# Performance work log

Hardware: AMD Instinct MI355X
Metric: run time of the kernel (lower is better)

The kernel has to match this reference:

```python
import jax, jax.numpy as jnp
import numpy as np


def _gumbel(key, shape):
    # -log(Exp(1)) == standard Gumbel; matches torch's -empty.exponential_().log()
    u = jax.random.uniform(key, shape, minval=1e-10, maxval=1.0)
    return -jnp.log(-jnp.log(u))


def setup_inputs() -> dict:
    key = jax.random.key(0)
    dims = [(1026, 1024), (3074, 1024), (5122, 512)]
    names = ['wc1', 'wc2', 'wd1', 'wd2', 'gc1', 'gc2', 'gd1', 'gd2']
    inp = {}
    k = key
    for li, (din, dout) in enumerate(dims, start=1):
        for nm in names:
            k, sub = jax.random.split(k)
            if nm.startswith('w'):
                inp[f'l{li}_{nm}'] = jax.random.normal(sub, (din, dout), dtype=jnp.float32)
            else:
                inp[f'l{li}_{nm}'] = _gumbel(sub, (din, dout)).astype(jnp.float32)
    k, kx, kw = jax.random.split(k, 3)
    inp['x'] = jax.random.uniform(kx, (32768, 512), dtype=jnp.float32)
    inp['lin_w'] = jax.random.uniform(kw, (1, 1024), dtype=jnp.float32)
    inp['tau'] = 1
    return inp


def _st_gate(w, g, tau):
    # hard gumbel-softmax over axis 0 with straight-through estimator
    y = jax.nn.softmax((w + g) / tau, axis=0)
    hard = jax.nn.one_hot(jnp.argmax(y, axis=0), w.shape[0], dtype=y.dtype).T
    return hard + y - jax.lax.stop_gradient(y)


def _logic_layer(h, ws, gs, tau, skip):
    wc1, wc2, wd1, wd2 = ws
    gc1, gc2, gd1, gd2 = gs
    c = (h @ _st_gate(wc1, gc1, tau)) * (h @ _st_gate(wc2, gc2, tau))  # AND
    a = h @ _st_gate(wd1, gd1, tau)
    b = h @ _st_gate(wd2, gd2, tau)
    d = 1.0 - (1.0 - a) * (1.0 - b)  # OR
    parts = [h, c, d] if skip else [c, d]
    return jnp.concatenate(parts, axis=-1)


def reference(x, l1_wc1, l1_wc2, l1_wd1, l1_wd2, l1_gc1, l1_gc2, l1_gd1, l1_gd2,
              l2_wc1, l2_wc2, l2_wd1, l2_wd2, l2_gc1, l2_gc2, l2_gd1, l2_gd2,
              l3_wc1, l3_wc2, l3_wd1, l3_wd2, l3_gc1, l3_gc2, l3_gd1, l3_gd2,
              lin_w, tau):
    t = jnp.asarray(tau, dtype=x.dtype)
    B = x.shape[0]
    # InputAugmentor: [x, 1-x, 1, 0]
    h = jnp.concatenate([x, 1.0 - x, jnp.ones((B, 1), x.dtype), jnp.zeros((B, 1), x.dtype)], axis=-1)
    layers = [
        ((l1_wc1, l1_wc2, l1_wd1, l1_wd2), (l1_gc1, l1_gc2, l1_gd1, l1_gd2), True),
        ((l2_wc1, l2_wc2, l2_wd1, l2_wd2), (l2_gc1, l2_gc2, l2_gd1, l2_gd2), True),
        ((l3_wc1, l3_wc2, l3_wd1, l3_wd2), (l3_gc1, l3_gc2, l3_gd1, l3_gd2), False),
    ]
    for ws, gs, skip in layers:
        h = _logic_layer(h, ws, gs, t, skip)
    # nonnegative == False -> weight used as-is
    return (h @ lin_w.T).squeeze(-1)
```

## Files before the change

### kernel.cpp

```cpp
#include <hip/hip_runtime.h>
#include <stdint.h>


struct GatePtrs {
    const float* w[12];
    const float* g[12];
};

__global__ __launch_bounds__(256) void argmax_kernel(GatePtrs gp,
                                                     unsigned long long* __restrict__ packed) {
    const int dins[3]  = {1026, 3074, 5122};
    const int douts[3] = {1024, 1024, 512};
    const int offs[3]  = {0, 4096, 8192};
    int gate  = blockIdx.z;
    int layer = gate >> 2;
    int din  = dins[layer];
    int dout = douts[layer];
    int c2 = blockIdx.x * 256 + threadIdx.x;
    int r0 = blockIdx.y * 64;
    if (2 * c2 >= dout || r0 >= din) return;
    int r1 = min(r0 + 64, din);
    const float* __restrict__ w = gp.w[gate];
    const float* __restrict__ g = gp.g[gate];
    float bx = -3.4e38f, by = -3.4e38f;
    int rx = r0, ry = r0;
    #pragma unroll 8
    for (int i = r0; i < r1; ++i) {
        float2 wv = *(const float2*)(w + (size_t)i * dout + 2 * c2);
        float2 gv = *(const float2*)(g + (size_t)i * dout + 2 * c2);
        float vx = wv.x + gv.x, vy = wv.y + gv.y;
        if (vx > bx) { bx = vx; rx = i; }
        if (vy > by) { by = vy; ry = i; }
    }
    unsigned long long* dst = packed + offs[layer] + (gate & 3) * dout + 2 * c2;
    unsigned int ux = __float_as_uint(bx);
    unsigned int kx = ux ^ ((ux & 0x80000000u) ? 0xFFFFFFFFu : 0x80000000u);
    atomicMax(dst, ((unsigned long long)kx << 32)
                   | (unsigned long long)(0xFFFFFFFFu - (unsigned int)rx));
    unsigned int uy = __float_as_uint(by);
    unsigned int ky = uy ^ ((uy & 0x80000000u) ? 0xFFFFFFFFu : 0x80000000u);
    atomicMax(dst + 1, ((unsigned long long)ky << 32)
                   | (unsigned long long)(0xFFFFFFFFu - (unsigned int)ry));
}

__global__ __launch_bounds__(256) void convert_kernel(const unsigned long long* __restrict__ packed,
                                                      uint2* __restrict__ pairs) {
    int i = blockIdx.x * 256 + threadIdx.x;
    if (i >= 5120) return;
    int l    = (i < 2048) ? 0 : ((i < 4096) ? 1 : 2);
    int half = (l == 2) ? 512 : 1024;
    int r    = i - l * 2048;
    int type = (r >= half) ? 1 : 0;
    int g    = r - type * half;
    int o1   = l * 4096 + 2 * type * half + g;
    int o2   = o1 + half;
    unsigned int i1 = 0xFFFFFFFFu - (unsigned int)(packed[o1] & 0xFFFFFFFFull);
    unsigned int i2 = 0xFFFFFFFFu - (unsigned int)(packed[o2] & 0xFFFFFFFFull);
    pairs[i] = make_uint2(i1 * 8u, i2 * 8u);
}

__global__ __launch_bounds__(512) void forward_kernel(const float* __restrict__ x,
                                                      const float* __restrict__ lin_w,
                                                      const uint2* __restrict__ pairs,
                                                      float* __restrict__ out) {
    __shared__ float2 hp[5122];
    __shared__ float2 red[8];
    const int t  = threadIdx.x;
    const int r0 = blockIdx.x * 2;
    const char* hb = (const char*)hp;

    float xa = x[(size_t)r0 * 512 + t];
    float xb = x[(size_t)(r0 + 1) * 512 + t];
    uint2 pa0 = pairs[t], pa1 = pairs[512 + t];
    uint2 po0 = pairs[1024 + t], po1 = pairs[1536 + t];
    hp[t]       = make_float2(xa, xb);
    hp[512 + t] = make_float2(1.0f - xa, 1.0f - xb);
    if (t == 0) { hp[1024] = make_float2(1.0f, 1.0f); hp[1025] = make_float2(0.0f, 0.0f); }
    __syncthreads();

    {
        float2 a0 = *(const float2*)(hb + pa0.x), b0 = *(const float2*)(hb + pa0.y);
        float2 a1 = *(const float2*)(hb + pa1.x), b1 = *(const float2*)(hb + pa1.y);
        float2 e0 = *(const float2*)(hb + po0.x), f0 = *(const float2*)(hb + po0.y);
        float2 e1 = *(const float2*)(hb + po1.x), f1 = *(const float2*)(hb + po1.y);
        hp[1026 + t]       = make_float2(a0.x * b0.x, a0.y * b0.y);
        hp[1538 + t]       = make_float2(a1.x * b1.x, a1.y * b1.y);
        hp[2050 + t]       = make_float2(1.0f - (1.0f - e0.x) * (1.0f - f0.x),
                                         1.0f - (1.0f - e0.y) * (1.0f - f0.y));
        hp[2562 + t]       = make_float2(1.0f - (1.0f - e1.x) * (1.0f - f1.x),
                                         1.0f - (1.0f - e1.y) * (1.0f - f1.y));
    }
    uint2 qa0 = pairs[2048 + t], qa1 = pairs[2560 + t];
    uint2 qo0 = pairs[3072 + t], qo1 = pairs[3584 + t];
    __syncthreads();

    {
        float2 a0 = *(const float2*)(hb + qa0.x), b0 = *(const float2*)(hb + qa0.y);
        float2 a1 = *(const float2*)(hb + qa1.x), b1 = *(const float2*)(hb + qa1.y);
        float2 e0 = *(const float2*)(hb + qo0.x), f0 = *(const float2*)(hb + qo0.y);
        float2 e1 = *(const float2*)(hb + qo1.x), f1 = *(const float2*)(hb + qo1.y);
        hp[3074 + t]       = make_float2(a0.x * b0.x, a0.y * b0.y);
        hp[3586 + t]       = make_float2(a1.x * b1.x, a1.y * b1.y);
        hp[4098 + t]       = make_float2(1.0f - (1.0f - e0.x) * (1.0f - f0.x),
                                         1.0f - (1.0f - e0.y) * (1.0f - f0.y));
        hp[4610 + t]       = make_float2(1.0f - (1.0f - e1.x) * (1.0f - f1.x),
                                         1.0f - (1.0f - e1.y) * (1.0f - f1.y));
    }
    uint2 za = pairs[4096 + t], zo = pairs[4608 + t];
    float wA = lin_w[t], wO = lin_w[512 + t];
    __syncthreads();

    float2 s;
    {
        float2 a = *(const float2*)(hb + za.x), b = *(const float2*)(hb + za.y);
        float2 e = *(const float2*)(hb + zo.x), f = *(const float2*)(hb + zo.y);
        float cx = a.x * b.x, cy = a.y * b.y;
        float dx = 1.0f - (1.0f - e.x) * (1.0f - f.x);
        float dy = 1.0f - (1.0f - e.y) * (1.0f - f.y);
        s.x = wA * cx + wO * dx;
        s.y = wA * cy + wO * dy;
    }

    #pragma unroll
    for (int off = 32; off > 0; off >>= 1) {
        s.x += __shfl_down(s.x, off, 64);
        s.y += __shfl_down(s.y, off, 64);
    }
    if ((t & 63) == 0) red[t >> 6] = s;
    __syncthreads();
    if (t == 0) {
        float2 tot = red[0];
        #pragma unroll
        for (int i = 1; i < 8; ++i) { tot.x += red[i].x; tot.y += red[i].y; }
        *(float2*)(out + r0) = tot;
    }
}

extern "C" void kernel_launch(void* const* d_in, const int* in_sizes, int n_in,
                              void* d_out, int out_size, void* d_ws, size_t ws_size,
                              hipStream_t stream) {
    GatePtrs gp;
    for (int l = 0; l < 3; ++l) {
        for (int s = 0; s < 4; ++s) {
            gp.w[l * 4 + s] = (const float*)d_in[l * 8 + s];
            gp.g[l * 4 + s] = (const float*)d_in[l * 8 + 4 + s];
        }
    }
    const float* x     = (const float*)d_in[24];
    const float* lin_w = (const float*)d_in[25];
    float* out = (float*)d_out;

    unsigned long long* packed = (unsigned long long*)d_ws;
    uint2* pairs = (uint2*)((char*)d_ws + 10240 * sizeof(unsigned long long));

    hipMemsetAsync(d_ws, 0, 10240 * sizeof(unsigned long long), stream);

    dim3 gridA(2 , 81 , 12 );
    argmax_kernel<<<gridA, 256, 0, stream>>>(gp, packed);

    convert_kernel<<<20, 256, 0, stream>>>(packed, pairs);

    forward_kernel<<<16384, 512, 0, stream>>>(x, lin_w, pairs, out);
}
```

Before: 368.8 us.

## Use fp16 packed activations, 4 rows per block, and two-pass argmax without atomics

The forward kernel now keeps activations in shared memory as half2 pairs, processes 4 batch rows per block instead of 2, and uses packed half math for the AND/OR gates. Gate indices are stored as 16-bit values. When enough workspace is available, the argmax is split into a partial pass with float4 loads over 16-row chunks and a separate reduction kernel, which replaces the memset and the 64-bit atomics. Computing in fp16 loses precision compared with the fp32 reference, so the output may drift from the expected tolerance.

```diff
diff --git a/kernel.cpp b/kernel.cpp
--- a/kernel.cpp
+++ b/kernel.cpp
@@ -1,4 +1,5 @@
 #include <hip/hip_runtime.h>
+#include <hip/hip_fp16.h>
 #include <stdint.h>
 
 
@@ -7,15 +8,83 @@
     const float* g[12];
 };
 
-__global__ __launch_bounds__(256) void argmax_kernel(GatePtrs gp,
+__device__ __forceinline__ unsigned int sortkey(float f) {
+    unsigned int u = __float_as_uint(f);
+    return u ^ ((u & 0x80000000u) ? 0xFFFFFFFFu : 0x80000000u);
+}
+
+__global__ __launch_bounds__(256) void argmax_part(GatePtrs gp,
+                                                   unsigned long long* __restrict__ part) {
+    const int dins[3]  = {1026, 3074, 5122};
+    const int douts[3] = {1024, 1024, 512};
+    const int chs[3]   = {65, 193, 321};
+    const int pbs[3]   = {0, 266240, 1056768};
+    int gate = blockIdx.z, layer = gate >> 2, slot = gate & 3;
+    int din = dins[layer], dout = douts[layer], ch = chs[layer];
+    int cols4 = dout >> 2;
+    int sub   = threadIdx.x / cols4;
+    int c4    = threadIdx.x - sub * cols4;
+    int chunk = blockIdx.y * (256 / cols4) + sub;
+    if (chunk >= ch) return;
+    int r0 = chunk * 16;
+    int r1 = min(r0 + 16, din);
+    const float* __restrict__ w = gp.w[gate] + (size_t)r0 * dout + 4 * c4;
+    const float* __restrict__ g = gp.g[gate] + (size_t)r0 * dout + 4 * c4;
+    float bx = -3.4e38f, by = bx, bz = bx, bw = bx;
+    int ix = r0, iy = r0, iz = r0, iw = r0;
+    #pragma unroll 8
+    for (int i = r0; i < r1; ++i) {
+        float4 wv = *(const float4*)w;
+        float4 gv = *(const float4*)g;
+        w += dout; g += dout;
+        float vx = wv.x + gv.x, vy = wv.y + gv.y;
+        float vz = wv.z + gv.z, vw = wv.w + gv.w;
+        if (vx > bx) { bx = vx; ix = i; }
+        if (vy > by) { by = vy; iy = i; }
+        if (vz > bz) { bz = vz; iz = i; }
+        if (vw > bw) { bw = vw; iw = i; }
+    }
+    unsigned long long* dst = part + pbs[layer]
+                            + ((size_t)(slot * ch + chunk)) * dout + 4 * c4;
+    dst[0] = ((unsigned long long)sortkey(bx) << 32) | (unsigned int)ix;
+    dst[1] = ((unsigned long long)sortkey(by) << 32) | (unsigned int)iy;
+    dst[2] = ((unsigned long long)sortkey(bz) << 32) | (unsigned int)iz;
+    dst[3] = ((unsigned long long)sortkey(bw) << 32) | (unsigned int)iw;
+}
+
+__global__ __launch_bounds__(256) void reduce_pairs(const unsigned long long* __restrict__ part,
+                                                    unsigned short* __restrict__ pf) {
+    int j = blockIdx.x * 256 + threadIdx.x;
+    if (j >= 10240) return;
+    int i = j >> 1, e = j & 1;
+    int l    = (i < 2048) ? 0 : ((i < 4096) ? 1 : 2);
+    int half = (l == 2) ? 512 : 1024;
+    int r    = i - l * 2048;
+    int type = (r >= half) ? 1 : 0;
+    int g    = r - type * half;
+    int s    = 2 * type + e;
+    const int chs[3] = {65, 193, 321};
+    const int pbs[3] = {0, 266240, 1056768};
+    const int dts[3] = {1024, 1024, 512};
+    int ch = chs[l], dout = dts[l];
+    const unsigned long long* p = part + pbs[l] + (size_t)s * ch * dout + g;
+    unsigned int bk = 0, brw = 0;
+    #pragma unroll 8
+    for (int c = 0; c < ch; ++c) {
+        unsigned long long v = p[(size_t)c * dout];
+        unsigned int k = (unsigned int)(v >> 32);
+        if (k > bk) { bk = k; brw = (unsigned int)v; }
+    }
+    pf[j] = (unsigned short)brw;
+}
+
+__global__ __launch_bounds__(256) void argmax_atomic(GatePtrs gp,
                                                      unsigned long long* __restrict__ packed) {
     const int dins[3]  = {1026, 3074, 5122};
     const int douts[3] = {1024, 1024, 512};
     const int offs[3]  = {0, 4096, 8192};
-    int gate  = blockIdx.z;
-    int layer = gate >> 2;
-    int din  = dins[layer];
-    int dout = douts[layer];
+    int gate = blockIdx.z, layer = gate >> 2;
+    int din = dins[layer], dout = douts[layer];
     int c2 = blockIdx.x * 256 + threadIdx.x;
     int r0 = blockIdx.y * 64;
     if (2 * c2 >= dout || r0 >= din) return;
@@ -33,18 +102,14 @@
         if (vy > by) { by = vy; ry = i; }
     }
     unsigned long long* dst = packed + offs[layer] + (gate & 3) * dout + 2 * c2;
-    unsigned int ux = __float_as_uint(bx);
-    unsigned int kx = ux ^ ((ux & 0x80000000u) ? 0xFFFFFFFFu : 0x80000000u);
-    atomicMax(dst, ((unsigned long long)kx << 32)
+    atomicMax(dst, ((unsigned long long)sortkey(bx) << 32)
                    | (unsigned long long)(0xFFFFFFFFu - (unsigned int)rx));
-    unsigned int uy = __float_as_uint(by);
-    unsigned int ky = uy ^ ((uy & 0x80000000u) ? 0xFFFFFFFFu : 0x80000000u);
-    atomicMax(dst + 1, ((unsigned long long)ky << 32)
+    atomicMax(dst + 1, ((unsigned long long)sortkey(by) << 32)
                    | (unsigned long long)(0xFFFFFFFFu - (unsigned int)ry));
 }
 
-__global__ __launch_bounds__(256) void convert_kernel(const unsigned long long* __restrict__ packed,
-                                                      uint2* __restrict__ pairs) {
+__global__ __launch_bounds__(256) void convert_fb(const unsigned long long* __restrict__ packed,
+                                                  ushort2* __restrict__ pf) {
     int i = blockIdx.x * 256 + threadIdx.x;
     if (i >= 5120) return;
     int l    = (i < 2048) ? 0 : ((i < 4096) ? 1 : 2);
@@ -56,83 +121,102 @@
     int o2   = o1 + half;
     unsigned int i1 = 0xFFFFFFFFu - (unsigned int)(packed[o1] & 0xFFFFFFFFull);
     unsigned int i2 = 0xFFFFFFFFu - (unsigned int)(packed[o2] & 0xFFFFFFFFull);
-    pairs[i] = make_uint2(i1 * 8u, i2 * 8u);
+    pf[i] = make_ushort2((unsigned short)i1, (unsigned short)i2);
+}
+
+__device__ __forceinline__ __half2 bc(unsigned int u) { return __builtin_bit_cast(__half2, u); }
+__device__ __forceinline__ unsigned int cb(__half2 h) { return __builtin_bit_cast(unsigned int, h); }
+
+__device__ __forceinline__ uint2 gat(const char* hb, unsigned int s) {
+    return *(const uint2*)(hb + (s << 3));
+}
+__device__ __forceinline__ uint2 andg(uint2 a, uint2 b) {
+    return make_uint2(cb(__hmul2(bc(a.x), bc(b.x))), cb(__hmul2(bc(a.y), bc(b.y))));
+}
+__device__ __forceinline__ uint2 org(uint2 a, uint2 b) {
+    __half2 one = __float2half2_rn(1.0f);
+    __half2 lo = __hsub2(one, __hmul2(__hsub2(one, bc(a.x)), __hsub2(one, bc(b.x))));
+    __half2 hi = __hsub2(one, __hmul2(__hsub2(one, bc(a.y)), __hsub2(one, bc(b.y))));
+    return make_uint2(cb(lo), cb(hi));
 }
 
 __global__ __launch_bounds__(512) void forward_kernel(const float* __restrict__ x,
                                                       const float* __restrict__ lin_w,
-                                                      const uint2* __restrict__ pairs,
+                                                      const ushort2* __restrict__ pairs,
                                                       float* __restrict__ out) {
-    __shared__ float2 hp[5122];
-    __shared__ float2 red[8];
+    __shared__ uint2 h[5122];
+    __shared__ float4 red[8];
     const int t  = threadIdx.x;
-    const int r0 = blockIdx.x * 2;
-    const char* hb = (const char*)hp;
-
-    float xa = x[(size_t)r0 * 512 + t];
+    const int r0 = blockIdx.x * 4;
+    const char* hb = (const char*)h;
+
+    float xa = x[(size_t)(r0 + 0) * 512 + t];
     float xb = x[(size_t)(r0 + 1) * 512 + t];
-    uint2 pa0 = pairs[t], pa1 = pairs[512 + t];
-    uint2 po0 = pairs[1024 + t], po1 = pairs[1536 + t];
-    hp[t]       = make_float2(xa, xb);
-    hp[512 + t] = make_float2(1.0f - xa, 1.0f - xb);
-    if (t == 0) { hp[1024] = make_float2(1.0f, 1.0f); hp[1025] = make_float2(0.0f, 0.0f); }
+    float xc = x[(size_t)(r0 + 2) * 512 + t];
+    float xd = x[(size_t)(r0 + 3) * 512 + t];
+    ushort2 pa0 = pairs[t], pa1 = pairs[512 + t];
+    ushort2 po0 = pairs[1024 + t], po1 = pairs[1536 + t];
+    h[t]       = make_uint2(cb(__floats2half2_rn(xa, xb)), cb(__floats2half2_rn(xc, xd)));
+    h[512 + t] = make_uint2(cb(__floats2half2_rn(1.f - xa, 1.f - xb)),
+                            cb(__floats2half2_rn(1.f - xc, 1.f - xd)));
+    if (t == 0) {
+        unsigned int o = cb(__float2half2_rn(1.0f));
+        h[1024] = make_uint2(o, o);
+        h[1025] = make_uint2(0u, 0u);
+    }
     __syncthreads();
 
     {
-        float2 a0 = *(const float2*)(hb + pa0.x), b0 = *(const float2*)(hb + pa0.y);
-        float2 a1 = *(const float2*)(hb + pa1.x), b1 = *(const float2*)(hb + pa1.y);
-        float2 e0 = *(const float2*)(hb + po0.x), f0 = *(const float2*)(hb + po0.y);
-        float2 e1 = *(const float2*)(hb + po1.x), f1 = *(const float2*)(hb + po1.y);
-        hp[1026 + t]       = make_float2(a0.x * b0.x, a0.y * b0.y);
-        hp[1538 + t]       = make_float2(a1.x * b1.x, a1.y * b1.y);
-        hp[2050 + t]       = make_float2(1.0f - (1.0f - e0.x) * (1.0f - f0.x),
-                                         1.0f - (1.0f - e0.y) * (1.0f - f0.y));
-        hp[2562 + t]       = make_float2(1.0f - (1.0f - e1.x) * (1.0f - f1.x),
-                                         1.0f - (1.0f - e1.y) * (1.0f - f1.y));
-    }
-    uint2 qa0 = pairs[2048 + t], qa1 = pairs[2560 + t];
-    uint2 qo0 = pairs[3072 + t], qo1 = pairs[3584 + t];
+        uint2 a0 = andg(gat(hb, pa0.x), gat(hb, pa0.y));
+        uint2 a1 = andg(gat(hb, pa1.x), gat(hb, pa1.y));
+        uint2 o0 = org(gat(hb, po0.x), gat(hb, po0.y));
+        uint2 o1 = org(gat(hb, po1.x), gat(hb, po1.y));
+        h[1026 + t] = a0; h[1538 + t] = a1;
+        h[2050 + t] = o0; h[2562 + t] = o1;
+    }
+    ushort2 qa0 = pairs[2048 + t], qa1 = pairs[2560 + t];
+    ushort2 qo0 = pairs[3072 + t], qo1 = pairs[3584 + t];
     __syncthreads();
 
     {
-        float2 a0 = *(const float2*)(hb + qa0.x), b0 = *(const float2*)(hb + qa0.y);
-        float2 a1 = *(const float2*)(hb + qa1.x), b1 = *(const float2*)(hb + qa1.y);
-        float2 e0 = *(const float2*)(hb + qo0.x), f0 = *(const float2*)(hb + qo0.y);
-        float2 e1 = *(const float2*)(hb + qo1.x), f1 = *(const float2*)(hb + qo1.y);
-        hp[3074 + t]       = make_float2(a0.x * b0.x, a0.y * b0.y);
-        hp[3586 + t]       = make_float2(a1.x * b1.x, a1.y * b1.y);
-        hp[4098 + t]       = make_float2(1.0f - (1.0f - e0.x) * (1.0f - f0.x),
-                                         1.0f - (1.0f - e0.y) * (1.0f - f0.y));
-        hp[4610 + t]       = make_float2(1.0f - (1.0f - e1.x) * (1.0f - f1.x),
-                                         1.0f - (1.0f - e1.y) * (1.0f - f1.y));
-    }
-    uint2 za = pairs[4096 + t], zo = pairs[4608 + t];
+        uint2 a0 = andg(gat(hb, qa0.x), gat(hb, qa0.y));
+        uint2 a1 = andg(gat(hb, qa1.x), gat(hb, qa1.y));
+        uint2 o0 = org(gat(hb, qo0.x), gat(hb, qo0.y));
+        uint2 o1 = org(gat(hb, qo1.x), gat(hb, qo1.y));
+        h[3074 + t] = a0; h[3586 + t] = a1;
+        h[4098 + t] = o0; h[4610 + t] = o1;
+    }
+    ushort2 za = pairs[4096 + t], zo = pairs[4608 + t];
     float wA = lin_w[t], wO = lin_w[512 + t];
     __syncthreads();
 
-    float2 s;
-    {
-        float2 a = *(const float2*)(hb + za.x), b = *(const float2*)(hb + za.y);
-        float2 e = *(const float2*)(hb + zo.x), f = *(const float2*)(hb + zo.y);
-        float cx = a.x * b.x, cy = a.y * b.y;
-        float dx = 1.0f - (1.0f - e.x) * (1.0f - f.x);
-        float dy = 1.0f - (1.0f - e.y) * (1.0f - f.y);
-        s.x = wA * cx + wO * dx;
-        s.y = wA * cy + wO * dy;
-    }
+    uint2 cg = andg(gat(hb, za.x), gat(hb, za.y));
+    uint2 dg = org(gat(hb, zo.x), gat(hb, zo.y));
+    float2 cl = __half22float2(bc(cg.x)), ch2 = __half22float2(bc(cg.y));
+    float2 dl = __half22float2(bc(dg.x)), dh = __half22float2(bc(dg.y));
+    float4 s;
+    s.x = wA * cl.x  + wO * dl.x;
+    s.y = wA * cl.y  + wO * dl.y;
+    s.z = wA * ch2.x + wO * dh.x;
+    s.w = wA * ch2.y + wO * dh.y;
 
     #pragma unroll
     for (int off = 32; off > 0; off >>= 1) {
         s.x += __shfl_down(s.x, off, 64);
         s.y += __shfl_down(s.y, off, 64);
+        s.z += __shfl_down(s.z, off, 64);
+        s.w += __shfl_down(s.w, off, 64);
     }
     if ((t & 63) == 0) red[t >> 6] = s;
     __syncthreads();
     if (t == 0) {
-        float2 tot = red[0];
+        float4 tot = red[0];
         #pragma unroll
-        for (int i = 1; i < 8; ++i) { tot.x += red[i].x; tot.y += red[i].y; }
-        *(float2*)(out + r0) = tot;
+        for (int i = 1; i < 8; ++i) {
+            tot.x += red[i].x; tot.y += red[i].y;
+            tot.z += red[i].z; tot.w += red[i].w;
+        }
+        *(float4*)(out + r0) = tot;
     }
 }
 
@@ -140,25 +224,30 @@
                               void* d_out, int out_size, void* d_ws, size_t ws_size,
                               hipStream_t stream) {
     GatePtrs gp;
-    for (int l = 0; l < 3; ++l) {
+    for (int l = 0; l < 3; ++l)
         for (int s = 0; s < 4; ++s) {
             gp.w[l * 4 + s] = (const float*)d_in[l * 8 + s];
             gp.g[l * 4 + s] = (const float*)d_in[l * 8 + 4 + s];
         }
-    }
     const float* x     = (const float*)d_in[24];
     const float* lin_w = (const float*)d_in[25];
     float* out = (float*)d_out;
 
-    unsigned long long* packed = (unsigned long long*)d_ws;
-    uint2* pairs = (uint2*)((char*)d_ws + 10240 * sizeof(unsigned long long));
-
-    hipMemsetAsync(d_ws, 0, 10240 * sizeof(unsigned long long), stream);
-
-    dim3 gridA(2 , 81 , 12 );
-    argmax_kernel<<<gridA, 256, 0, stream>>>(gp, packed);
-
-    convert_kernel<<<20, 256, 0, stream>>>(packed, pairs);
-
-    forward_kernel<<<16384, 512, 0, stream>>>(x, lin_w, pairs, out);
-}
+    const size_t partBytes = 1714176ull * 8ull;
+    if (ws_size >= partBytes + 20480) {
+        unsigned long long* part = (unsigned long long*)d_ws;
+        unsigned short* pf = (unsigned short*)((char*)d_ws + partBytes);
+        dim3 ga(1, 193, 12);
+        argmax_part<<<ga, 256, 0, stream>>>(gp, part);
+        reduce_pairs<<<40, 256, 0, stream>>>(part, pf);
+        forward_kernel<<<8192, 512, 0, stream>>>(x, lin_w, (const ushort2*)pf, out);
+    } else {
+        unsigned long long* packed = (unsigned long long*)d_ws;
+        ushort2* pf = (ushort2*)((char*)d_ws + 10240 * 8);
+        hipMemsetAsync(d_ws, 0, 10240 * 8, stream);
+        dim3 ga(2, 81, 12);
+        argmax_atomic<<<ga, 256, 0, stream>>>(gp, packed);
+        convert_fb<<<20, 256, 0, stream>>>(packed, pf);
+        forward_kernel<<<8192, 512, 0, stream>>>(x, lin_w, (const ushort2*)pf, out);
+    }
+}
```

After: 353.1 us. -4.2%, faster.
